# Kernel optimization log

Hardware: AMD Instinct MI355X
Metric: run time of the kernel (lower is better)

The kernel has to match this reference:

```python
import math
import jax, jax.numpy as jnp
import numpy as np

IN_CH = 64
NUM_ANCHOR = 4
MAP_H, MAP_W = 96, 96
BATCH = 8
BN_EPS = 1e-5


def _conv2d(x, w, b, padding, dilation):
    # x: [B,C,H,W], w: [O,I,kh,kw] (OIHW)
    y = jax.lax.conv_general_dilated(
        x, w, window_strides=(1, 1),
        padding=((padding, padding), (padding, padding)),
        rhs_dilation=(dilation, dilation),
        dimension_numbers=('NCHW', 'OIHW', 'NCHW'))
    return y + b[None, :, None, None]


def _bn(x, gamma, beta, mean, var):
    scale = gamma / jnp.sqrt(var + BN_EPS)
    return x * scale[None, :, None, None] + (beta - mean * scale)[None, :, None, None]


def setup_inputs() -> dict:
    key = jax.random.key(0)
    ks = jax.random.split(key, 12)
    # cyclic channel-shift permutation matrices, one per anchor pass
    eye = np.eye(IN_CH, dtype=np.float32)
    shift = IN_CH // (2 * NUM_ANCHOR)
    perms = np.stack([eye[np.roll(np.arange(IN_CH), i * shift)] for i in range(2 * NUM_ANCHOR)])
    w_std = 1.0 / math.sqrt(IN_CH * 9)
    return {
        'x': jax.random.normal(ks[0], (BATCH, IN_CH, MAP_H, MAP_W), dtype=jnp.float32),
        'perms': jnp.asarray(perms),
        'dcn_w': jax.random.normal(ks[1], (IN_CH, IN_CH, 3, 3), dtype=jnp.float32) * w_std,
        'dcn_b': jax.random.normal(ks[2], (IN_CH,), dtype=jnp.float32) * 0.01,
        'conv2_w': jax.random.normal(ks[3], (IN_CH, IN_CH, 3, 3), dtype=jnp.float32) * w_std,
        'conv2_b': jax.random.normal(ks[4], (IN_CH,), dtype=jnp.float32) * 0.01,
        'conv3_w': jax.random.normal(ks[5], (IN_CH, IN_CH, 3, 3), dtype=jnp.float32) * w_std,
        'conv3_b': jax.random.normal(ks[6], (IN_CH,), dtype=jnp.float32) * 0.01,
        'bn_gamma': jax.random.uniform(ks[7], (3, IN_CH), dtype=jnp.float32, minval=0.5, maxval=1.5),
        'bn_beta': jax.random.normal(ks[8], (3, IN_CH), dtype=jnp.float32) * 0.1,
        'bn_mean': jax.random.normal(ks[9], (3, IN_CH), dtype=jnp.float32) * 0.1,
        'bn_var': jax.random.uniform(ks[10], (3, IN_CH), dtype=jnp.float32, minval=0.5, maxval=1.5),
    }


def reference(x, perms, dcn_w, dcn_b, conv2_w, conv2_b, conv3_w, conv3_b,
              bn_gamma, bn_beta, bn_mean, bn_var):
    h = x.shape[2]
    pad = math.ceil(h / (2 ** 1.5 + 2))  # 20 for h=96

    def conv_stack(o):
        # DCN at init (zero offsets) == plain 3x3 conv, pad=1
        o = jax.nn.relu(_bn(_conv2d(o, dcn_w, dcn_b, 1, 1), bn_gamma[0], bn_beta[0], bn_mean[0], bn_var[0]))
        o = jax.nn.relu(_bn(_conv2d(o, conv2_w, conv2_b, 2, 2), bn_gamma[1], bn_beta[1], bn_mean[1], bn_var[1]))
        o = jax.nn.relu(_bn(_conv2d(o, conv3_w, conv3_b, 2, 2), bn_gamma[2], bn_beta[2], bn_mean[2], bn_var[2]))
        return o

    outs = []
    for i in range(2 * NUM_ANCHOR):  # fixed small structural loop
        o = jnp.einsum('mn,bnhw->bmhw', perms[i], x)  # channel permutation
        if i % 2 != 0:
            o = jnp.pad(o, ((0, 0), (0, 0), (pad, pad), (pad, pad)))
        o = jnp.rot90(o, k=i % 4, axes=(-2, -1))   # ccw rotate
        o = conv_stack(o)
        o = jnp.rot90(o, k=(-i) % 4, axes=(-2, -1))  # cw rotate back
        if i % 2 != 0:
            H, W = o.shape[-2], o.shape[-1]
            sh, sw = (H - MAP_H) // 2, (W - MAP_W) // 2
            o = o[..., sh:sh + MAP_H, sw:sw + MAP_W]  # center crop
        outs.append(o)
    out_tensor = jnp.concatenate(outs, axis=1)  # [B, 8*C, H, W]
    out = jnp.max(out_tensor, axis=1, keepdims=True)
    # branch_name == 'midpoint', orientational_anchor=False -> clamped sigmoid
    return jnp.clip(jax.nn.sigmoid(out), 1e-4, 1.0 - 1e-4)
```

## Files before the change

### kernel.cpp

```cpp
#include <hip/hip_runtime.h>
#include <math.h>

#define B 8
#define C 64
#define HW 96
#define NWV 36864

typedef __attribute__((ext_vector_type(8)))  short short8;
typedef __attribute__((ext_vector_type(16))) float floatx16;

__device__ __forceinline__ unsigned short f2bf(float f) {
    unsigned int u = __float_as_uint(f);
    unsigned int r = (u + 0x7fffu + ((u >> 16) & 1u)) >> 16;
    return (unsigned short)r;
}

__device__ __forceinline__ void rotmap(int k, int ta, int tb, int& sa, int& sb) {
    switch (k) {
        case 0: sa = ta;     sb = tb;     break;
        case 1: sa = 2 - tb; sb = ta;     break;
        case 2: sa = 2 - ta; sb = 2 - tb; break;
        default: sa = tb;    sb = 2 - ta; break;
    }
}

__global__ void prep_w(const float* __restrict__ dcn_w, const float* __restrict__ c2w,
                       const float* __restrict__ c3w,
                       const float* __restrict__ gamma, const float* __restrict__ var_,
                       unsigned short* __restrict__ Wall) {
    int idx = blockIdx.x * 256 + threadIdx.x;
    if (idx >= 16 * NWV) return;
    int v = idx / NWV, rem = idx % NWV;
    int tap  = rem >> 12;
    int w12  = rem & 4095;
    int ks   = w12 >> 10;
    int cf   = (w12 >> 9) & 1;
    int lane = (w12 >> 3) & 63;
    int j    = w12 & 7;
    int co = cf * 32 + (lane & 31);
    int ci = ks * 16 + (lane >> 5) * 8 + j;
    int ta = tap / 3, tb = tap % 3;
    const float* src; int k, srcci, l;
    if (v < 8)       { k = v & 3;  srcci = (ci + 8 * v) & 63; src = dcn_w; l = 0; }
    else if (v < 12) { k = v - 8;  srcci = ci; src = c2w; l = 1; }
    else             { k = v - 12; srcci = ci; src = c3w; l = 2; }
    int sa, sb; rotmap(k, ta, tb, sa, sb);
    float s = gamma[l * 64 + co] * rsqrtf(var_[l * 64 + co] + 1e-5f);
    Wall[idx] = f2bf(src[((co * 64 + srcci) * 3 + sa) * 3 + sb] * s);
}

__global__ void prep_bias(const float* __restrict__ dcn_b, const float* __restrict__ c2b,
                          const float* __restrict__ c3b,
                          const float* __restrict__ gamma, const float* __restrict__ beta,
                          const float* __restrict__ mean, const float* __restrict__ var_,
                          float* __restrict__ biasg) {
    int t = threadIdx.x;
    if (t < 192) {
        int l = t >> 6, c = t & 63;
        const float* cb = (l == 0) ? dcn_b : ((l == 1) ? c2b : c3b);
        float s = gamma[l * 64 + c] * rsqrtf(var_[l * 64 + c] + 1e-5f);
        biasg[t] = cb[c] * s + beta[l * 64 + c] - mean[l * 64 + c] * s;
    }
}

__global__ __launch_bounds__(256) void prep_x(const float* __restrict__ in,
                                              unsigned short* __restrict__ out) {
    __shared__ float row[64 * 97];
    int by = blockIdx.x;
    int b = by / 96, y = by % 96;
    int t = threadIdx.x;
    for (int e = t; e < 6144; e += 256) {
        int c = e / 96, x = e - c * 96;
        row[c * 97 + x] = in[(((size_t)(b * 64 + c) * 96 + y) * 96) + x];
    }
    __syncthreads();
    for (int e = t; e < 6144; e += 256) {
        int x = e >> 6, c = e & 63;
        out[(((size_t)(b * 96 + y) * 96 + x) << 6) + c] = f2bf(row[c * 97 + x]);
    }
}

__global__ __launch_bounds__(256) void border_clear(unsigned short* __restrict__ buf1) {
    int idx = blockIdx.y;
    int br = (idx >> 3) * 2, b = idx & 7;
    int z = br * 8 + b;
    int i = blockIdx.x * 32 + (threadIdx.x >> 3);
    int g = threadIdx.x & 7;
    int r, c;
    if (i < 416)      { r = i / 104;              c = i % 104; }
    else if (i < 832) { int j = i - 416; r = 100 + j / 104; c = j % 104; }
    else              { int j = i - 832; r = 4 + (j >> 3); int c8 = j & 7;
                        c = (c8 < 4) ? c8 : 92 + c8; }
    uint4 zero = make_uint4(0u, 0u, 0u, 0u);
    *(uint4*)(buf1 + (size_t)z * (104 * 104 * 64) + ((size_t)(r * 104 + c) << 6) + (g << 3)) = zero;
}

__global__ __launch_bounds__(256, 2) void conv1_k(
    const unsigned short* __restrict__ xhwc, unsigned short* __restrict__ buf1,
    const unsigned short* __restrict__ Wall, const float* __restrict__ biasg) {

    __shared__ __align__(16) unsigned short xt[10 * 34 * 64];

    int z = blockIdx.z, br = z >> 3, b = z & 7, odd = br & 1;
    int fy0 = blockIdx.y * 8, fx0 = blockIdx.x * 32;
    int t = threadIdx.x, lane = t & 63, wv = t >> 6;
    int n = lane & 31, kq = lane >> 5;

    const unsigned short* xb = xhwc + ((size_t)b * 96 * 96 << 6);
    const short8* Ag = (const short8*)(Wall + (size_t)br * NWV);

    for (int e = t; e < 2720; e += 256) {
        int p = e >> 3, g = e & 7;
        int yy = p / 34, xx = p - yy * 34;
        int gy = fy0 - 5 + yy, gx = fx0 - 5 + xx;
        uint4 v = make_uint4(0u, 0u, 0u, 0u);
        if ((unsigned)gy < 96u && (unsigned)gx < 96u)
            v = *(const uint4*)(xb + ((size_t)(gy * 96 + gx) << 6) + (g << 3));
        *(uint4*)(xt + (p << 6) + ((g ^ (xx & 7)) << 3)) = v;
    }
    __syncthreads();

    floatx16 acc[2][2];
#pragma unroll
    for (int cf = 0; cf < 2; cf++)
#pragma unroll
        for (int pf = 0; pf < 2; pf++)
#pragma unroll
            for (int i = 0; i < 16; i++) acc[cf][pf][i] = 0.f;

#pragma unroll
    for (int ks = 0; ks < 4; ks++) {
#pragma unroll
        for (int tb = 0; tb < 3; tb++) {
            short8 a[3][2];
#pragma unroll
            for (int ta = 0; ta < 3; ta++)
#pragma unroll
                for (int cf = 0; cf < 2; cf++)
                    a[ta][cf] = Ag[(((ta * 3 + tb) * 4 + ks) * 2 + cf) * 64 + lane];
            int xx = n + tb;
            int g = ((ks * 2 + kq) ^ (xx & 7)) << 3;
            short8 bf[4];
#pragma unroll
            for (int rr = 0; rr < 4; rr++) {
                int p = (2 * wv + rr) * 34 + xx;
                bf[rr] = *(const short8*)(xt + (p << 6) + g);
            }
#pragma unroll
            for (int ta = 0; ta < 3; ta++)
#pragma unroll
                for (int pf = 0; pf < 2; pf++) {
                    int rr = pf + ta;
                    acc[0][pf] = __builtin_amdgcn_mfma_f32_32x32x16_bf16(a[ta][0], bf[rr], acc[0][pf], 0, 0, 0);
                    acc[1][pf] = __builtin_amdgcn_mfma_f32_32x32x16_bf16(a[ta][1], bf[rr], acc[1][pf], 0, 0, 0);
                }
        }
    }

    float4 bv[2][4];
#pragma unroll
    for (int cf = 0; cf < 2; cf++)
#pragma unroll
        for (int rb = 0; rb < 4; rb++)
            bv[cf][rb] = *(const float4*)(biasg + 32 * cf + 8 * rb + 4 * kq);

    __syncthreads();
#pragma unroll
    for (int pf = 0; pf < 2; pf++) {
        int pq = (2 * wv + pf) * 32 + n;
        int key = (pq & 7) << 1;
#pragma unroll
        for (int cf = 0; cf < 2; cf++)
#pragma unroll
            for (int rb = 0; rb < 4; rb++) {
                int u = kq + 2 * rb + 8 * cf;
                float v0 = fmaxf(acc[cf][pf][rb * 4 + 0] + bv[cf][rb].x, 0.f);
                float v1 = fmaxf(acc[cf][pf][rb * 4 + 1] + bv[cf][rb].y, 0.f);
                float v2 = fmaxf(acc[cf][pf][rb * 4 + 2] + bv[cf][rb].z, 0.f);
                float v3 = fmaxf(acc[cf][pf][rb * 4 + 3] + bv[cf][rb].w, 0.f);
                uint2 pk = make_uint2((unsigned)f2bf(v0) | ((unsigned)f2bf(v1) << 16),
                                      (unsigned)f2bf(v2) | ((unsigned)f2bf(v3) << 16));
                *(uint2*)((char*)xt + pq * 128 + ((u ^ key) << 3)) = pk;
            }
    }
    __syncthreads();

    unsigned short* fb = buf1 + (size_t)z * (104 * 104 * 64);
    int lo = odd ? 0 : 4, hi = odd ? 104 : 100;
    for (int e = t; e < 2048; e += 256) {
        int px = e >> 3, g = e & 7;
        int key = (px & 7) << 1;
        uint4 v = *(const uint4*)((const char*)xt + px * 128 + (((2 * g) ^ key) << 3));
        int lr = px >> 5, nn = px & 31;
        int f = fy0 + lr, fc = fx0 + nn;
        if (f >= lo && f < hi && fc >= lo && fc < hi)
            *(uint4*)(fb + ((size_t)(f * 104 + fc) << 6) + (g << 3)) = v;
    }
}

__global__ __launch_bounds__(512, 2) void conv23_k(
    const unsigned short* __restrict__ buf1, float* __restrict__ maxb,
    const unsigned short* __restrict__ Wall, const float* __restrict__ biasg) {

    __shared__ __align__(16) unsigned char ubuf[768 * 144];
    unsigned short* xs = (unsigned short*)ubuf;
    char* c2out = (char*)ubuf;

    int z = blockIdx.z, br = z >> 3, odd = br & 1;
    int oy0 = blockIdx.y * 16, ox0 = blockIdx.x * 32;
    int t = threadIdx.x, lane = t & 63, wv = t >> 6;
    int n = lane & 31, kq = lane >> 5;

    const unsigned short* fb = buf1 + (size_t)z * (104 * 104 * 64);
    const short8* A2 = (const short8*)(Wall + (size_t)(8  + (br & 3)) * NWV);
    const short8* A3 = (const short8*)(Wall + (size_t)(12 + (br & 3)) * NWV);

    for (int e = t; e < 3840; e += 512) {
        int p = e >> 2, g = e & 3;
        int yy = p / 40, xx = p - yy * 40;
        uint4 v = *(const uint4*)(fb + ((size_t)((oy0 + yy) * 104 + ox0 + xx) << 6) + (g << 3));
        *(uint4*)(xs + (p << 5) + ((g ^ (xx & 3)) << 3)) = v;
    }
    __syncthreads();

    uint4 pfv[8];
#pragma unroll
    for (int k = 0; k < 8; k++) {
        int e = t + k * 512;
        if (e < 3840) {
            int p = e >> 2, g = e & 3;
            int yy = p / 40, xx = p - yy * 40;
            pfv[k] = *(const uint4*)(fb + ((size_t)((oy0 + yy) * 104 + ox0 + xx) << 6) + 32 + (g << 3));
        }
    }

    int q_[3], row2_[3], col2_[3];
#pragma unroll
    for (int jj = 0; jj < 3; jj++) {
        int q = 96 * wv + 32 * jj + n;
        q_[jj] = q;
        int qc = (q < 720) ? q : 719;
        int r2 = qc / 36;
        row2_[jj] = r2;
        col2_[jj] = qc - 36 * r2;
    }

    floatx16 acc2[3][2];
#pragma unroll
    for (int jj = 0; jj < 3; jj++)
#pragma unroll
        for (int cf = 0; cf < 2; cf++)
#pragma unroll
            for (int i = 0; i < 16; i++) acc2[jj][cf][i] = 0.f;

#pragma unroll
    for (int s = 0; s < 2; s++) {
        if (s == 1) {
            __syncthreads();
#pragma unroll
            for (int k = 0; k < 8; k++) {
                int e = t + k * 512;
                if (e < 3840) {
                    int p = e >> 2, g = e & 3;
                    int xx2 = p - (p / 40) * 40;
                    *(uint4*)(xs + (p << 5) + ((g ^ (xx2 & 3)) << 3)) = pfv[k];
                }
            }
            __syncthreads();
        }
#pragma unroll
        for (int kl = 0; kl < 2; kl++) {
            int ks = s * 2 + kl;
#pragma unroll
            for (int tb = 0; tb < 3; tb++) {
                short8 a[3][2];
#pragma unroll
                for (int ta = 0; ta < 3; ta++)
#pragma unroll
                    for (int cf = 0; cf < 2; cf++)
                        a[ta][cf] = A2[(((ta * 3 + tb) * 4 + ks) * 2 + cf) * 64 + lane];
#pragma unroll
                for (int jj = 0; jj < 3; jj++) {
                    int colx = col2_[jj] + 2 * tb;
                    int gsw = ((kl * 2 + kq) ^ (colx & 3)) << 3;
#pragma unroll
                    for (int ta = 0; ta < 3; ta++) {
                        int p = (row2_[jj] + 2 * ta) * 40 + colx;
                        short8 bfr = *(const short8*)(xs + (p << 5) + gsw);
                        acc2[jj][0] = __builtin_amdgcn_mfma_f32_32x32x16_bf16(a[ta][0], bfr, acc2[jj][0], 0, 0, 0);
                        acc2[jj][1] = __builtin_amdgcn_mfma_f32_32x32x16_bf16(a[ta][1], bfr, acc2[jj][1], 0, 0, 0);
                    }
                }
            }
        }
    }

    __syncthreads();

    int rlo2 = (!odd && oy0 == 0)  ? 2  : 0;
    int rhi2 = (!odd && oy0 == 80) ? 18 : 20;
    int clo2 = (!odd && ox0 == 0)  ? 2  : 0;
    int chi2 = (!odd && ox0 == 64) ? 34 : 36;
    float4 bv2[2][4];
#pragma unroll
    for (int cf = 0; cf < 2; cf++)
#pragma unroll
        for (int rb = 0; rb < 4; rb++)
            bv2[cf][rb] = *(const float4*)(biasg + 64 + 32 * cf + 8 * rb + 4 * kq);

#pragma unroll
    for (int jj = 0; jj < 3; jj++) {
        if (q_[jj] < 720) {
            bool valid = (row2_[jj] >= rlo2) && (row2_[jj] < rhi2) &&
                         (col2_[jj] >= clo2) && (col2_[jj] < chi2);
            int key = col2_[jj] & 14;
#pragma unroll
            for (int cf = 0; cf < 2; cf++)
#pragma unroll
                for (int rb = 0; rb < 4; rb++) {
                    int u = kq + 2 * rb + 8 * cf;
                    float v0 = 0.f, v1 = 0.f, v2 = 0.f, v3 = 0.f;
                    if (valid) {
                        v0 = fmaxf(acc2[jj][cf][rb * 4 + 0] + bv2[cf][rb].x, 0.f);
                        v1 = fmaxf(acc2[jj][cf][rb * 4 + 1] + bv2[cf][rb].y, 0.f);
                        v2 = fmaxf(acc2[jj][cf][rb * 4 + 2] + bv2[cf][rb].z, 0.f);
                        v3 = fmaxf(acc2[jj][cf][rb * 4 + 3] + bv2[cf][rb].w, 0.f);
                    }
                    uint2 pk = make_uint2((unsigned)f2bf(v0) | ((unsigned)f2bf(v1) << 16),
                                          (unsigned)f2bf(v2) | ((unsigned)f2bf(v3) << 16));
                    *(uint2*)(c2out + q_[jj] * 144 + ((u ^ key) << 3)) = pk;
                }
        }
    }
    __syncthreads();

    int r0 = 2 * wv;
    floatx16 acc3[2][2];
#pragma unroll
    for (int cf = 0; cf < 2; cf++)
#pragma unroll
        for (int pf = 0; pf < 2; pf++)
#pragma unroll
            for (int i = 0; i < 16; i++) acc3[cf][pf][i] = 0.f;

#pragma unroll
    for (int ks = 0; ks < 4; ks++) {
#pragma unroll
        for (int tb = 0; tb < 3; tb++) {
            short8 a[3][2];
#pragma unroll
            for (int ta = 0; ta < 3; ta++)
#pragma unroll
                for (int cf = 0; cf < 2; cf++)
                    a[ta][cf] = A3[(((ta * 3 + tb) * 4 + ks) * 2 + cf) * 64 + lane];
            int col = n + 2 * tb;
            int key = col & 14;
            int ublk = 2 * (ks * 2 + kq);
            short8 bf[6];
#pragma unroll
            for (int rr = 0; rr < 6; rr++) {
                int q = (r0 + rr) * 36 + col;
                bf[rr] = *(const short8*)(c2out + q * 144 + ((ublk ^ key) << 3));
            }
#pragma unroll
            for (int ta = 0; ta < 3; ta++)
#pragma unroll
                for (int pf = 0; pf < 2; pf++) {
                    int rr = pf + 2 * ta;
                    acc3[0][pf] = __builtin_amdgcn_mfma_f32_32x32x16_bf16(a[ta][0], bf[rr], acc3[0][pf], 0, 0, 0);
                    acc3[1][pf] = __builtin_amdgcn_mfma_f32_32x32x16_bf16(a[ta][1], bf[rr], acc3[1][pf], 0, 0, 0);
                }
        }
    }

    float4 bv3[2][4];
#pragma unroll
    for (int cf = 0; cf < 2; cf++)
#pragma unroll
        for (int rb = 0; rb < 4; rb++)
            bv3[cf][rb] = *(const float4*)(biasg + 128 + 32 * cf + 8 * rb + 4 * kq);

#pragma unroll
    for (int pf = 0; pf < 2; pf++) {
        float m = 0.f;
#pragma unroll
        for (int cf = 0; cf < 2; cf++)
#pragma unroll
            for (int rb = 0; rb < 4; rb++) {
                m = fmaxf(m, acc3[cf][pf][rb * 4 + 0] + bv3[cf][rb].x);
                m = fmaxf(m, acc3[cf][pf][rb * 4 + 1] + bv3[cf][rb].y);
                m = fmaxf(m, acc3[cf][pf][rb * 4 + 2] + bv3[cf][rb].z);
                m = fmaxf(m, acc3[cf][pf][rb * 4 + 3] + bv3[cf][rb].w);
            }
        m = fmaxf(m, 0.f);
        m = fmaxf(m, __shfl_xor(m, 32, 64));
        if (lane < 32)
            maxb[((size_t)z * 96 + oy0 + r0 + pf) * 96 + ox0 + n] = m;
    }
}

__global__ void final_k(const float* __restrict__ maxb, float* __restrict__ out) {
    int i = blockIdx.x * 256 + threadIdx.x;
    if (i < B * HW * HW) {
        int b = i / 9216, yx = i - b * 9216;
        float m = 0.f;
#pragma unroll
        for (int br = 0; br < 8; br++)
            m = fmaxf(m, maxb[((size_t)(br * 8 + b)) * 9216 + yx]);
        float v = 1.f / (1.f + expf(-m));
        out[i] = fminf(fmaxf(v, 1e-4f), 1.f - 1e-4f);
    }
}


extern "C" void kernel_launch(void* const* d_in, const int* in_sizes, int n_in,
                              void* d_out, int out_size, void* d_ws, size_t ws_size,
                              hipStream_t stream) {
    const float* x     = (const float*)d_in[0];
    const float* dcn_w = (const float*)d_in[2];
    const float* dcn_b = (const float*)d_in[3];
    const float* c2w   = (const float*)d_in[4];
    const float* c2b   = (const float*)d_in[5];
    const float* c3w   = (const float*)d_in[6];
    const float* c3b   = (const float*)d_in[7];
    const float* gamma = (const float*)d_in[8];
    const float* beta  = (const float*)d_in[9];
    const float* mean  = (const float*)d_in[10];
    const float* var_  = (const float*)d_in[11];

    char* ws = (char*)d_ws;
    unsigned short* Wall = (unsigned short*)ws;
    size_t off = (size_t)16 * NWV * 2;
    float* biasg = (float*)(ws + off);            off += 1024;
    float* maxb  = (float*)(ws + off);            off += (size_t)64 * 9216 * 4;
    unsigned short* xhwc = (unsigned short*)(ws + off); off += (size_t)B * 9216 * 64 * 2;
    unsigned short* buf1 = (unsigned short*)(ws + off);

    prep_w<<<(16 * NWV + 255) / 256, 256, 0, stream>>>(dcn_w, c2w, c3w, gamma, var_, Wall);
    prep_bias<<<1, 256, 0, stream>>>(dcn_b, c2b, c3b, gamma, beta, mean, var_, biasg);
    prep_x<<<B * 96, 256, 0, stream>>>(x, xhwc);
    border_clear<<<dim3(50, 32), 256, 0, stream>>>(buf1);

    dim3 g1(4, 13, 64);
    conv1_k<<<g1, 256, 0, stream>>>(xhwc, buf1, Wall, biasg);

    dim3 g23(3, 6, 64);
    conv23_k<<<g23, 512, 0, stream>>>(buf1, maxb, Wall, biasg);

    final_k<<<(B * HW * HW + 255) / 256, 256, 0, stream>>>(maxb, (float*)d_out);
}
```

Baseline: 311.8 us.

## Stage conv weights through double-buffered LDS and load full-channel input tile at once

The fused conv2/conv3 kernel now stages each K-slice of the conv2 and conv3 weights into a double-buffered LDS area, prefetching the next slice into registers while the current one feeds the MFMAs. This replaces per-lane global weight loads. The input tile is loaded with all 64 channels at once using a wider swizzle, which removes the two-stage half-channel reload and its extra barriers. The price is more LDS per block (about 156KB including the weight buffers), which may cut the two-blocks-per-CU occupancy, plus a barrier on every K step.

```diff
diff --git a/kernel.cpp b/kernel.cpp
--- a/kernel.cpp
+++ b/kernel.cpp
@@ -198,11 +198,28 @@
     }
 }
 
+#define WLOAD(src, ksv)                                                              \
+    _Pragma("unroll")                                                                \
+    for (int k2 = 0; k2 < 3; k2++) {                                                 \
+        int e = t + k2 * 512;                                                        \
+        if (e < 1152) {                                                              \
+            int f = e >> 6, c = e & 63;                                              \
+            wr[k2] = *(const uint4*)((src) + (((f >> 1) * 4 + (ksv)) * 2 + (f & 1)) * 512 + c * 8); \
+        }                                                                            \
+    }
+#define WSTORE(bufidx)                                                               \
+    _Pragma("unroll")                                                                \
+    for (int k2 = 0; k2 < 3; k2++) {                                                 \
+        int e = t + k2 * 512;                                                        \
+        if (e < 1152) *(uint4*)(&wlds[bufidx][e << 4]) = wr[k2];                     \
+    }
+
 __global__ __launch_bounds__(512, 2) void conv23_k(
     const unsigned short* __restrict__ buf1, float* __restrict__ maxb,
     const unsigned short* __restrict__ Wall, const float* __restrict__ biasg) {
 
-    __shared__ __align__(16) unsigned char ubuf[768 * 144];
+    __shared__ __align__(16) unsigned char ubuf[960 * 128];
+    __shared__ __align__(16) unsigned char wlds[2][18432];
     unsigned short* xs = (unsigned short*)ubuf;
     char* c2out = (char*)ubuf;
 
@@ -212,27 +229,20 @@
     int n = lane & 31, kq = lane >> 5;
 
     const unsigned short* fb = buf1 + (size_t)z * (104 * 104 * 64);
-    const short8* A2 = (const short8*)(Wall + (size_t)(8  + (br & 3)) * NWV);
-    const short8* A3 = (const short8*)(Wall + (size_t)(12 + (br & 3)) * NWV);
-
-    for (int e = t; e < 3840; e += 512) {
-        int p = e >> 2, g = e & 3;
+    const unsigned short* A2g = Wall + (size_t)(8  + (br & 3)) * NWV;
+    const unsigned short* A3g = Wall + (size_t)(12 + (br & 3)) * NWV;
+
+    for (int e = t; e < 7680; e += 512) {
+        int p = e >> 3, g = e & 7;
         int yy = p / 40, xx = p - yy * 40;
         uint4 v = *(const uint4*)(fb + ((size_t)((oy0 + yy) * 104 + ox0 + xx) << 6) + (g << 3));
-        *(uint4*)(xs + (p << 5) + ((g ^ (xx & 3)) << 3)) = v;
-    }
-    __syncthreads();
-
-    uint4 pfv[8];
-#pragma unroll
-    for (int k = 0; k < 8; k++) {
-        int e = t + k * 512;
-        if (e < 3840) {
-            int p = e >> 2, g = e & 3;
-            int yy = p / 40, xx = p - yy * 40;
-            pfv[k] = *(const uint4*)(fb + ((size_t)((oy0 + yy) * 104 + ox0 + xx) << 6) + 32 + (g << 3));
-        }
-    }
+        *(uint4*)(xs + (p << 6) + ((g ^ (xx & 7)) << 3)) = v;
+    }
+
+    uint4 wr[3];
+    WLOAD(A2g, 0)
+    WSTORE(0)
+    WLOAD(A2g, 1)
 
     int q_[3], row2_[3], col2_[3];
 #pragma unroll
@@ -253,49 +263,37 @@
 #pragma unroll
             for (int i = 0; i < 16; i++) acc2[jj][cf][i] = 0.f;
 
-#pragma unroll
-    for (int s = 0; s < 2; s++) {
-        if (s == 1) {
-            __syncthreads();
-#pragma unroll
-            for (int k = 0; k < 8; k++) {
-                int e = t + k * 512;
-                if (e < 3840) {
-                    int p = e >> 2, g = e & 3;
-                    int xx2 = p - (p / 40) * 40;
-                    *(uint4*)(xs + (p << 5) + ((g ^ (xx2 & 3)) << 3)) = pfv[k];
-                }
-            }
-            __syncthreads();
-        }
-#pragma unroll
-        for (int kl = 0; kl < 2; kl++) {
-            int ks = s * 2 + kl;
-#pragma unroll
-            for (int tb = 0; tb < 3; tb++) {
-                short8 a[3][2];
-#pragma unroll
-                for (int ta = 0; ta < 3; ta++)
-#pragma unroll
-                    for (int cf = 0; cf < 2; cf++)
-                        a[ta][cf] = A2[(((ta * 3 + tb) * 4 + ks) * 2 + cf) * 64 + lane];
-#pragma unroll
-                for (int jj = 0; jj < 3; jj++) {
-                    int colx = col2_[jj] + 2 * tb;
-                    int gsw = ((kl * 2 + kq) ^ (colx & 3)) << 3;
-#pragma unroll
-                    for (int ta = 0; ta < 3; ta++) {
-                        int p = (row2_[jj] + 2 * ta) * 40 + colx;
-                        short8 bfr = *(const short8*)(xs + (p << 5) + gsw);
-                        acc2[jj][0] = __builtin_amdgcn_mfma_f32_32x32x16_bf16(a[ta][0], bfr, acc2[jj][0], 0, 0, 0);
-                        acc2[jj][1] = __builtin_amdgcn_mfma_f32_32x32x16_bf16(a[ta][1], bfr, acc2[jj][1], 0, 0, 0);
-                    }
+    __syncthreads();
+
+#pragma unroll
+    for (int ks = 0; ks < 4; ks++) {
+        WSTORE((ks + 1) & 1)
+        if (ks < 2) { WLOAD(A2g, ks + 2) }
+        else        { WLOAD(A3g, ks - 2) }
+        const char* wq = (const char*)wlds[ks & 1];
+#pragma unroll
+        for (int tb = 0; tb < 3; tb++) {
+            short8 a[3][2];
+#pragma unroll
+            for (int ta = 0; ta < 3; ta++)
+#pragma unroll
+                for (int cf = 0; cf < 2; cf++)
+                    a[ta][cf] = *(const short8*)(wq + (((((ta * 3 + tb) * 2 + cf) << 6) | lane) << 4));
+#pragma unroll
+            for (int jj = 0; jj < 3; jj++) {
+                int colx = col2_[jj] + 2 * tb;
+                int gsw = ((ks * 2 + kq) ^ (colx & 7)) << 3;
+#pragma unroll
+                for (int ta = 0; ta < 3; ta++) {
+                    int p = (row2_[jj] + 2 * ta) * 40 + colx;
+                    short8 bfr = *(const short8*)(xs + (p << 6) + gsw);
+                    acc2[jj][0] = __builtin_amdgcn_mfma_f32_32x32x16_bf16(a[ta][0], bfr, acc2[jj][0], 0, 0, 0);
+                    acc2[jj][1] = __builtin_amdgcn_mfma_f32_32x32x16_bf16(a[ta][1], bfr, acc2[jj][1], 0, 0, 0);
                 }
             }
         }
-    }
-
-    __syncthreads();
+        __syncthreads();
+    }
 
     int rlo2 = (!odd && oy0 == 0)  ? 2  : 0;
     int rhi2 = (!odd && oy0 == 80) ? 18 : 20;
@@ -328,7 +326,7 @@
                     }
                     uint2 pk = make_uint2((unsigned)f2bf(v0) | ((unsigned)f2bf(v1) << 16),
                                           (unsigned)f2bf(v2) | ((unsigned)f2bf(v3) << 16));
-                    *(uint2*)(c2out + q_[jj] * 144 + ((u ^ key) << 3)) = pk;
+                    *(uint2*)(c2out + q_[jj] * 128 + ((u ^ key) << 3)) = pk;
                 }
         }
     }
@@ -345,6 +343,9 @@
 
 #pragma unroll
     for (int ks = 0; ks < 4; ks++) {
+        if (ks < 3) { WSTORE((ks + 1) & 1) }
+        if (ks < 2) { WLOAD(A3g, ks + 2) }
+        const char* wq = (const char*)wlds[ks & 1];
 #pragma unroll
         for (int tb = 0; tb < 3; tb++) {
             short8 a[3][2];
@@ -352,7 +353,7 @@
             for (int ta = 0; ta < 3; ta++)
 #pragma unroll
                 for (int cf = 0; cf < 2; cf++)
-                    a[ta][cf] = A3[(((ta * 3 + tb) * 4 + ks) * 2 + cf) * 64 + lane];
+                    a[ta][cf] = *(const short8*)(wq + (((((ta * 3 + tb) * 2 + cf) << 6) | lane) << 4));
             int col = n + 2 * tb;
             int key = col & 14;
             int ublk = 2 * (ks * 2 + kq);
@@ -360,7 +361,7 @@
 #pragma unroll
             for (int rr = 0; rr < 6; rr++) {
                 int q = (r0 + rr) * 36 + col;
-                bf[rr] = *(const short8*)(c2out + q * 144 + ((ublk ^ key) << 3));
+                bf[rr] = *(const short8*)(c2out + q * 128 + ((ublk ^ key) << 3));
             }
 #pragma unroll
             for (int ta = 0; ta < 3; ta++)
@@ -371,6 +372,7 @@
                     acc3[1][pf] = __builtin_amdgcn_mfma_f32_32x32x16_bf16(a[ta][1], bf[rr], acc3[1][pf], 0, 0, 0);
                 }
         }
+        if (ks < 3) __syncthreads();
     }
 
     float4 bv3[2][4];
```

After: 313.3 us. Within noise of the previous version (+0.5%).
